# Performance work log

Hardware: AMD Instinct MI355X
Metric: run time of the kernel (lower is better)

## Reference

```python
import jax, jax.numpy as jnp
import numpy as np

N_NODES = 200000
D = 128            # in_channels
B_GRAPHS = 512     # batch_size
STEPS = 3          # processing_steps


def setup_inputs() -> dict:
    key = jax.random.key(0)
    k = jax.random.split(key, 6)
    x = jax.random.normal(k[0], (N_NODES, D), dtype=jnp.float32)
    batch = jnp.sort(jax.random.randint(k[1], (N_NODES,), 0, B_GRAPHS, dtype=jnp.int64))
    s = 0.1
    W_ih = jax.random.normal(k[2], (3 * D, 2 * D), dtype=jnp.float32) * s
    W_hh = jax.random.normal(k[3], (3 * D, D), dtype=jnp.float32) * s
    b_ih = jax.random.normal(k[4], (3 * D,), dtype=jnp.float32) * s
    b_hh = jax.random.normal(k[5], (3 * D,), dtype=jnp.float32) * s
    return {"x": x, "batch": batch, "batch_size": B_GRAPHS,
            "W_ih": W_ih, "W_hh": W_hh, "b_ih": b_ih, "b_hh": b_hh}


def _gru_cell(inp, h, W_ih, W_hh, b_ih, b_hh):
    # inp: [B, 2d], h: [B, d]; PyTorch GRU gate order: r, z, n
    gi = inp @ W_ih.T + b_ih  # [B, 3d]
    gh = h @ W_hh.T + b_hh    # [B, 3d]
    gi_r, gi_z, gi_n = jnp.split(gi, 3, axis=-1)
    gh_r, gh_z, gh_n = jnp.split(gh, 3, axis=-1)
    r = jax.nn.sigmoid(gi_r + gh_r)
    z = jax.nn.sigmoid(gi_z + gh_z)
    n = jnp.tanh(gi_n + r * gh_n)
    return (1.0 - z) * n + z * h


def reference(x, batch, batch_size, W_ih, W_hh, b_ih, b_hh):
    B = batch_size
    d = x.shape[1]
    h = jnp.zeros((B, d), dtype=x.dtype)
    q_star = jnp.zeros((B, 2 * d), dtype=x.dtype)
    for _ in range(STEPS):
        h = _gru_cell(q_star, h, W_ih, W_hh, b_ih, b_hh)
        q = h  # num_layers=1: output == new hidden state
        e = jnp.sum(x * q[batch], axis=-1)  # [N]
        m = jax.ops.segment_max(e, batch, num_segments=B)
        ex = jnp.exp(e - m[batch])
        s = jax.ops.segment_sum(ex, batch, num_segments=B)
        a = ex / (s[batch] + 1e-16)  # segment softmax weights [N]
        r = jax.ops.segment_sum(a[:, None] * x, batch, num_segments=B)  # [B, d]
        q_star = jnp.concatenate([q, r], axis=-1)
    return q_star
```

## Files before the change

kernel.cpp:

```cpp
#include <hip/hip_runtime.h>
#include <math.h>
#include <float.h>

constexpr int D = 128;
constexpr int B = 512;
constexpr int STEPS = 3;
constexpr int NW_IH = 3 * D * 2 * D;
constexpr int NW_HH = 3 * D * D;
constexpr float NEG_HUGE = -3.402823466e38f;

__device__ __forceinline__ float sigmoidf_(float x) { return 1.f / (1.f + __expf(-x)); }
__device__ __forceinline__ float bflo(unsigned int u) { return __uint_as_float(u << 16); }
__device__ __forceinline__ float bfhi(unsigned int u) { return __uint_as_float(u & 0xffff0000u); }
__device__ __forceinline__ unsigned short f2bf_rn(float f) {
    unsigned int u = __float_as_uint(f);
    u += 0x7fffu + ((u >> 16) & 1u);
    return (unsigned short)(u >> 16);
}
__device__ __forceinline__ float4 ld4(const float* p) { return *(const float4*)p; }
__device__ __forceinline__ int imin_(int a, int b) { return a < b ? a : b; }

__global__ __launch_bounds__(256) void k_prep(const float* __restrict__ Wih,
        const float* __restrict__ Whh, const int* __restrict__ batch, int n,
        unsigned short* __restrict__ wih_bf, unsigned short* __restrict__ whh_bf,
        int* __restrict__ seg) {
    int i = blockIdx.x * blockDim.x + threadIdx.x;
    if (i < NW_IH) wih_bf[i] = f2bf_rn(Wih[i]);
    else if (i < NW_IH + NW_HH) whh_bf[i - NW_IH] = f2bf_rn(Whh[i - NW_IH]);
    if (i <= B) {
        int lo = 0, hi = n;
        while (lo < hi) { int mid = (lo + hi) >> 1; if (batch[mid] < i) lo = mid + 1; else hi = mid; }
        seg[i] = lo;
    }
}

struct Trip { float4 a0, a1, b0, b1, c0, c1, d0, d1; };

__global__ __launch_bounds__(256, 2) void k_set2set(
        const float* __restrict__ x,
        const unsigned short* __restrict__ wih_bf,
        const unsigned short* __restrict__ whh_bf,
        const float* __restrict__ bih, const float* __restrict__ bhh,
        const int* __restrict__ seg, float* __restrict__ out) {
    __shared__ __align__(16) float s_q[2 * D];
    __shared__ __align__(16) float s_h[D];
    __shared__ float s_gi[3 * D], s_gh[3 * D];
    __shared__ float sm[16], sl[16];
    __shared__ __align__(16) float rpart[4][D];

    const int b = blockIdx.x;
    const int tid = threadIdx.x;
    const int start = seg[b], end = seg[b + 1];
    const int g = tid >> 4;
    const int s = tid & 15;
    const int s8 = s * 8;

    const int len = end - start;
    const int FT = (len + 63) >> 6;
    const int gbase = start + g;
    const int eclamp = (len > 0) ? end - 1 : start;

    float m_run, l_run;
    float4 acc0, acc1;
    float4 q0, q1;
    Trip T0_, T1_, T2_, T3_;

    auto load_trip = [&](Trip& T, int t) {
        const int n0 = gbase + (t << 6);
        const float* p0 = x + ((size_t)imin_(n0,      eclamp) << 7) + s8;
        const float* p1 = x + ((size_t)imin_(n0 + 16, eclamp) << 7) + s8;
        const float* p2 = x + ((size_t)imin_(n0 + 32, eclamp) << 7) + s8;
        const float* p3 = x + ((size_t)imin_(n0 + 48, eclamp) << 7) + s8;
        T.a0 = ld4(p0); T.a1 = ld4(p0 + 4);
        T.b0 = ld4(p1); T.b1 = ld4(p1 + 4);
        T.c0 = ld4(p2); T.c1 = ld4(p2 + 4);
        T.d0 = ld4(p3); T.d1 = ld4(p3 + 4);
    };
    auto dot8 = [&](const float4& lo, const float4& hi) {
        float p = lo.x * q0.x;
        p = fmaf(lo.y, q0.y, p); p = fmaf(lo.z, q0.z, p); p = fmaf(lo.w, q0.w, p);
        p = fmaf(hi.x, q1.x, p); p = fmaf(hi.y, q1.y, p);
        p = fmaf(hi.z, q1.z, p); p = fmaf(hi.w, q1.w, p);
        return p;
    };
    auto compute_core = [&](const Trip& T, bool masked, int t) {
        float p0 = dot8(T.a0, T.a1);
        float p1 = dot8(T.b0, T.b1);
        float p2 = dot8(T.c0, T.c1);
        float p3 = dot8(T.d0, T.d1);
        p0 += __shfl_xor(p0, 1, 64); p1 += __shfl_xor(p1, 1, 64);
        p2 += __shfl_xor(p2, 1, 64); p3 += __shfl_xor(p3, 1, 64);
        p0 += __shfl_xor(p0, 2, 64); p1 += __shfl_xor(p1, 2, 64);
        p2 += __shfl_xor(p2, 2, 64); p3 += __shfl_xor(p3, 2, 64);
        p0 += __shfl_xor(p0, 4, 64); p1 += __shfl_xor(p1, 4, 64);
        p2 += __shfl_xor(p2, 4, 64); p3 += __shfl_xor(p3, 4, 64);
        p0 += __shfl_xor(p0, 8, 64); p1 += __shfl_xor(p1, 8, 64);
        p2 += __shfl_xor(p2, 8, 64); p3 += __shfl_xor(p3, 8, 64);
        bool m0 = true, m1 = true, m2 = true, m3 = true;
        float h0 = p0, h1 = p1, h2 = p2, h3 = p3;
        if (masked) {
            const int n0 = gbase + (t << 6);
            m0 = n0 < end; m1 = n0 + 16 < end; m2 = n0 + 32 < end; m3 = n0 + 48 < end;
            h0 = m0 ? p0 : NEG_HUGE; h1 = m1 ? p1 : NEG_HUGE;
            h2 = m2 ? p2 : NEG_HUGE; h3 = m3 ? p3 : NEG_HUGE;
        }
        float nm = fmaxf(m_run, fmaxf(fmaxf(h0, h1), fmaxf(h2, h3)));
        float sc = __expf(m_run - nm);
        float e0 = __expf(p0 - nm), e1 = __expf(p1 - nm);
        float e2 = __expf(p2 - nm), e3 = __expf(p3 - nm);
        if (masked) {
            e0 = m0 ? e0 : 0.f; e1 = m1 ? e1 : 0.f;
            e2 = m2 ? e2 : 0.f; e3 = m3 ? e3 : 0.f;
        }
        l_run = fmaf(l_run, sc, (e0 + e1) + (e2 + e3));
        acc0.x = fmaf(acc0.x, sc, fmaf(e0, T.a0.x, fmaf(e1, T.b0.x, fmaf(e2, T.c0.x, e3 * T.d0.x))));
        acc0.y = fmaf(acc0.y, sc, fmaf(e0, T.a0.y, fmaf(e1, T.b0.y, fmaf(e2, T.c0.y, e3 * T.d0.y))));
        acc0.z = fmaf(acc0.z, sc, fmaf(e0, T.a0.z, fmaf(e1, T.b0.z, fmaf(e2, T.c0.z, e3 * T.d0.z))));
        acc0.w = fmaf(acc0.w, sc, fmaf(e0, T.a0.w, fmaf(e1, T.b0.w, fmaf(e2, T.c0.w, e3 * T.d0.w))));
        acc1.x = fmaf(acc1.x, sc, fmaf(e0, T.a1.x, fmaf(e1, T.b1.x, fmaf(e2, T.c1.x, e3 * T.d1.x))));
        acc1.y = fmaf(acc1.y, sc, fmaf(e0, T.a1.y, fmaf(e1, T.b1.y, fmaf(e2, T.c1.y, e3 * T.d1.y))));
        acc1.z = fmaf(acc1.z, sc, fmaf(e0, T.a1.z, fmaf(e1, T.b1.z, fmaf(e2, T.c1.z, e3 * T.d1.z))));
        acc1.w = fmaf(acc1.w, sc, fmaf(e0, T.a1.w, fmaf(e1, T.b1.w, fmaf(e2, T.c1.w, e3 * T.d1.w))));
        m_run = nm;
    };
    auto compute  = [&](const Trip& T)        { compute_core(T, false, 0); };
    auto computeM = [&](const Trip& T, int t) { compute_core(T, true,  t); };

    if (FT > 0) load_trip(T0_, 0);
    if (FT > 1) load_trip(T1_, 1);
    if (FT > 2) load_trip(T2_, 2);
    if (FT > 3) load_trip(T3_, 3);

    if (tid < 2 * D) s_q[tid] = 0.f;
    if (tid < D) s_h[tid] = 0.f;
    __syncthreads();

    for (int step = 0; step < STEPS; ++step) {
        if (tid < 192) {
            const int r0 = tid * 2, r1 = r0 + 1;
            float gi0 = bih[r0], gi1 = bih[r1];
            float gh0 = bhh[r0], gh1 = bhh[r1];
            const float4* q4 = (const float4*)s_q;
            const float4* h4 = (const float4*)s_h;
            const uint4* w0 = (const uint4*)(wih_bf + (size_t)r0 * (2 * D));
            const uint4* w1 = (const uint4*)(wih_bf + (size_t)r1 * (2 * D));
#pragma unroll 4
            for (int c = 0; c < 32; ++c) {
                uint4 wa = w0[c], wb = w1[c];
                float4 qa = q4[2 * c], qb = q4[2 * c + 1];
                gi0 = fmaf(bflo(wa.x), qa.x, gi0); gi0 = fmaf(bfhi(wa.x), qa.y, gi0);
                gi0 = fmaf(bflo(wa.y), qa.z, gi0); gi0 = fmaf(bfhi(wa.y), qa.w, gi0);
                gi0 = fmaf(bflo(wa.z), qb.x, gi0); gi0 = fmaf(bfhi(wa.z), qb.y, gi0);
                gi0 = fmaf(bflo(wa.w), qb.z, gi0); gi0 = fmaf(bfhi(wa.w), qb.w, gi0);
                gi1 = fmaf(bflo(wb.x), qa.x, gi1); gi1 = fmaf(bfhi(wb.x), qa.y, gi1);
                gi1 = fmaf(bflo(wb.y), qa.z, gi1); gi1 = fmaf(bfhi(wb.y), qa.w, gi1);
                gi1 = fmaf(bflo(wb.z), qb.x, gi1); gi1 = fmaf(bfhi(wb.z), qb.y, gi1);
                gi1 = fmaf(bflo(wb.w), qb.z, gi1); gi1 = fmaf(bfhi(wb.w), qb.w, gi1);
            }
            const uint4* v0 = (const uint4*)(whh_bf + (size_t)r0 * D);
            const uint4* v1 = (const uint4*)(whh_bf + (size_t)r1 * D);
#pragma unroll 4
            for (int c = 0; c < 16; ++c) {
                uint4 wa = v0[c], wb = v1[c];
                float4 ha = h4[2 * c], hb = h4[2 * c + 1];
                gh0 = fmaf(bflo(wa.x), ha.x, gh0); gh0 = fmaf(bfhi(wa.x), ha.y, gh0);
                gh0 = fmaf(bflo(wa.y), ha.z, gh0); gh0 = fmaf(bfhi(wa.y), ha.w, gh0);
                gh0 = fmaf(bflo(wa.z), hb.x, gh0); gh0 = fmaf(bfhi(wa.z), hb.y, gh0);
                gh0 = fmaf(bflo(wa.w), hb.z, gh0); gh0 = fmaf(bfhi(wa.w), hb.w, gh0);
                gh1 = fmaf(bflo(wb.x), ha.x, gh1); gh1 = fmaf(bfhi(wb.x), ha.y, gh1);
                gh1 = fmaf(bflo(wb.y), ha.z, gh1); gh1 = fmaf(bfhi(wb.y), ha.w, gh1);
                gh1 = fmaf(bflo(wb.z), hb.x, gh1); gh1 = fmaf(bfhi(wb.z), hb.y, gh1);
                gh1 = fmaf(bflo(wb.w), hb.z, gh1); gh1 = fmaf(bfhi(wb.w), hb.w, gh1);
            }
            s_gi[r0] = gi0; s_gi[r1] = gi1;
            s_gh[r0] = gh0; s_gh[r1] = gh1;
        }
        __syncthreads();
        if (tid < D) {
            const int t = tid;
            float r  = sigmoidf_(s_gi[t] + s_gh[t]);
            float z  = sigmoidf_(s_gi[D + t] + s_gh[D + t]);
            float nn = tanhf(s_gi[2 * D + t] + r * s_gh[2 * D + t]);
            float hn = (1.f - z) * nn + z * s_h[t];
            s_h[t] = hn;
            s_q[t] = hn;
        }
        __syncthreads();

        q0 = ((const float4*)s_h)[2 * s];
        q1 = ((const float4*)s_h)[2 * s + 1];
        m_run = NEG_HUGE; l_run = 0.f;
        acc0 = make_float4(0.f, 0.f, 0.f, 0.f);
        acc1 = make_float4(0.f, 0.f, 0.f, 0.f);

        int t = 0;
        while (t + 8 <= FT) {
            compute(T0_); load_trip(T0_, t + 4);
            compute(T1_); load_trip(T1_, t + 5);
            compute(T2_); load_trip(T2_, t + 6);
            compute(T3_); load_trip(T3_, t + 7);
            t += 4;
        }
        int rem = FT - t;
        if (rem > 4) {
            compute(T0_); load_trip(T0_, t + 4);
            compute(T1_); if (rem > 5) load_trip(T1_, t + 5);
            compute(T2_); if (rem > 6) load_trip(T2_, t + 6);
            compute(T3_);
            t += 4; rem -= 4;
        }
        if (rem > 0) { if (t     == FT - 1) computeM(T0_, t);     else compute(T0_); }
        if (rem > 1) { if (t + 1 == FT - 1) computeM(T1_, t + 1); else compute(T1_); }
        if (rem > 2) { if (t + 2 == FT - 1) computeM(T2_, t + 2); else compute(T2_); }
        if (rem > 3) computeM(T3_, t + 3);

        if (step + 1 < STEPS) {
            if (FT > 0) load_trip(T0_, 0);
            if (FT > 1) load_trip(T1_, 1);
            if (FT > 2) load_trip(T2_, 2);
            if (FT > 3) load_trip(T3_, 3);
        }

        if (s == 0) { sm[g] = m_run; sl[g] = l_run; }
        __syncthreads();

        {
            const float mv = sm[s];
            const float lv = sl[s];
            float M = mv;
            M = fmaxf(M, __shfl_xor(M, 1, 64));
            M = fmaxf(M, __shfl_xor(M, 2, 64));
            M = fmaxf(M, __shfl_xor(M, 4, 64));
            M = fmaxf(M, __shfl_xor(M, 8, 64));
            float term = lv * __expf(mv - M);
            term += __shfl_xor(term, 1, 64);
            term += __shfl_xor(term, 2, 64);
            term += __shfl_xor(term, 4, 64);
            term += __shfl_xor(term, 8, 64);
            const float inv = 1.f / (term + 1e-16f);
            const float fac = __expf(m_run - M) * inv;
            acc0.x *= fac; acc0.y *= fac; acc0.z *= fac; acc0.w *= fac;
            acc1.x *= fac; acc1.y *= fac; acc1.z *= fac; acc1.w *= fac;
        }
        acc0.x += __shfl_xor(acc0.x, 16, 64); acc0.y += __shfl_xor(acc0.y, 16, 64);
        acc0.z += __shfl_xor(acc0.z, 16, 64); acc0.w += __shfl_xor(acc0.w, 16, 64);
        acc1.x += __shfl_xor(acc1.x, 16, 64); acc1.y += __shfl_xor(acc1.y, 16, 64);
        acc1.z += __shfl_xor(acc1.z, 16, 64); acc1.w += __shfl_xor(acc1.w, 16, 64);
        acc0.x += __shfl_xor(acc0.x, 32, 64); acc0.y += __shfl_xor(acc0.y, 32, 64);
        acc0.z += __shfl_xor(acc0.z, 32, 64); acc0.w += __shfl_xor(acc0.w, 32, 64);
        acc1.x += __shfl_xor(acc1.x, 32, 64); acc1.y += __shfl_xor(acc1.y, 32, 64);
        acc1.z += __shfl_xor(acc1.z, 32, 64); acc1.w += __shfl_xor(acc1.w, 32, 64);

        const int wv = tid >> 6;
        if ((tid & 63) < 16) {
            float4* dst = (float4*)&rpart[wv][s8];
            dst[0] = acc0; dst[1] = acc1;
        }
        __syncthreads();
        if (tid < D) {
            float v = (rpart[0][tid] + rpart[1][tid]) + (rpart[2][tid] + rpart[3][tid]);
            s_q[D + tid] = v;
        }
        __syncthreads();
    }

    if (tid < 2 * D) out[(size_t)b * (2 * D) + tid] = s_q[tid];
}

extern "C" void kernel_launch(void* const* d_in, const int* in_sizes, int n_in,
                              void* d_out, int out_size, void* d_ws, size_t ws_size,
                              hipStream_t stream) {
    const float* x    = (const float*)d_in[0];
    const int*   batch= (const int*)d_in[1];
    const float* Wih  = (const float*)d_in[3];
    const float* Whh  = (const float*)d_in[4];
    const float* bih  = (const float*)d_in[5];
    const float* bhh  = (const float*)d_in[6];
    const int n = in_sizes[0] / D;

    char* ws = (char*)d_ws;
    int* seg = (int*)ws;
    unsigned short* wih_bf = (unsigned short*)(ws + 4096);
    unsigned short* whh_bf = (unsigned short*)(ws + 4096 + (size_t)NW_IH * 2);

    const int total = NW_IH + NW_HH;
    k_prep<<<(total + 255) / 256, 256, 0, stream>>>(Wih, Whh, batch, n, wih_bf, whh_bf, seg);
    k_set2set<<<B, 256, 0, stream>>>(x, wih_bf, whh_bf, bih, bhh, seg, (float*)d_out);
}
```

Baseline: 268.3 us.

## Parallelize GRU matvec across all lanes, coalesce x loads, shrink prefetch depth

The GRU gate matvecs move from 192 threads each computing two full rows serially to all 256 threads, with half-wave or quarter-wave lanes splitting each row and reducing via shuffles. Biases are added in the elementwise stage. The x row loads switch from 8 contiguous floats per lane to two 16-byte loads 64 floats apart, so each load instruction is contiguous across lanes. The prefetch ring drops from four to two trips, freeing registers but exposing more memory latency on large segments, and the first trip is now loaded each step before the GRU instead of overlapped with the previous step's tail.

Result: slower. 335.0 us (+24.9%).

```diff
diff --git a/kernel.cpp b/kernel.cpp
--- a/kernel.cpp
+++ b/kernel.cpp
@@ -53,7 +53,7 @@
     const int start = seg[b], end = seg[b + 1];
     const int g = tid >> 4;
     const int s = tid & 15;
-    const int s8 = s * 8;
+    const int s4 = s * 4;
 
     const int len = end - start;
     const int FT = (len + 63) >> 6;
@@ -63,18 +63,18 @@
     float m_run, l_run;
     float4 acc0, acc1;
     float4 q0, q1;
-    Trip T0_, T1_, T2_, T3_;
+    Trip T0_, T1_;
 
     auto load_trip = [&](Trip& T, int t) {
         const int n0 = gbase + (t << 6);
-        const float* p0 = x + ((size_t)imin_(n0,      eclamp) << 7) + s8;
-        const float* p1 = x + ((size_t)imin_(n0 + 16, eclamp) << 7) + s8;
-        const float* p2 = x + ((size_t)imin_(n0 + 32, eclamp) << 7) + s8;
-        const float* p3 = x + ((size_t)imin_(n0 + 48, eclamp) << 7) + s8;
-        T.a0 = ld4(p0); T.a1 = ld4(p0 + 4);
-        T.b0 = ld4(p1); T.b1 = ld4(p1 + 4);
-        T.c0 = ld4(p2); T.c1 = ld4(p2 + 4);
-        T.d0 = ld4(p3); T.d1 = ld4(p3 + 4);
+        const float* p0 = x + ((size_t)imin_(n0,      eclamp) << 7) + s4;
+        const float* p1 = x + ((size_t)imin_(n0 + 16, eclamp) << 7) + s4;
+        const float* p2 = x + ((size_t)imin_(n0 + 32, eclamp) << 7) + s4;
+        const float* p3 = x + ((size_t)imin_(n0 + 48, eclamp) << 7) + s4;
+        T.a0 = ld4(p0); T.a1 = ld4(p0 + 64);
+        T.b0 = ld4(p1); T.b1 = ld4(p1 + 64);
+        T.c0 = ld4(p2); T.c1 = ld4(p2 + 64);
+        T.d0 = ld4(p3); T.d1 = ld4(p3 + 64);
     };
     auto dot8 = [&](const float4& lo, const float4& hi) {
         float p = lo.x * q0.x;
@@ -126,99 +126,98 @@
     auto compute  = [&](const Trip& T)        { compute_core(T, false, 0); };
     auto computeM = [&](const Trip& T, int t) { compute_core(T, true,  t); };
 
-    if (FT > 0) load_trip(T0_, 0);
-    if (FT > 1) load_trip(T1_, 1);
-    if (FT > 2) load_trip(T2_, 2);
-    if (FT > 3) load_trip(T3_, 3);
-
     if (tid < 2 * D) s_q[tid] = 0.f;
     if (tid < D) s_h[tid] = 0.f;
     __syncthreads();
 
+    const int wv   = tid >> 6;
+    const int l64  = tid & 63;
+    const int half = l64 >> 5, c32 = l64 & 31;
+    const int quarter = l64 >> 4, c16 = l64 & 15;
+    const int rb = wv * 96;
+
     for (int step = 0; step < STEPS; ++step) {
-        if (tid < 192) {
-            const int r0 = tid * 2, r1 = r0 + 1;
-            float gi0 = bih[r0], gi1 = bih[r1];
-            float gh0 = bhh[r0], gh1 = bhh[r1];
+        if (FT > 0) load_trip(T0_, 0);
+
+        {
             const float4* q4 = (const float4*)s_q;
             const float4* h4 = (const float4*)s_h;
-            const uint4* w0 = (const uint4*)(wih_bf + (size_t)r0 * (2 * D));
-            const uint4* w1 = (const uint4*)(wih_bf + (size_t)r1 * (2 * D));
-#pragma unroll 4
-            for (int c = 0; c < 32; ++c) {
-                uint4 wa = w0[c], wb = w1[c];
-                float4 qa = q4[2 * c], qb = q4[2 * c + 1];
-                gi0 = fmaf(bflo(wa.x), qa.x, gi0); gi0 = fmaf(bfhi(wa.x), qa.y, gi0);
-                gi0 = fmaf(bflo(wa.y), qa.z, gi0); gi0 = fmaf(bfhi(wa.y), qa.w, gi0);
-                gi0 = fmaf(bflo(wa.z), qb.x, gi0); gi0 = fmaf(bfhi(wa.z), qb.y, gi0);
-                gi0 = fmaf(bflo(wa.w), qb.z, gi0); gi0 = fmaf(bfhi(wa.w), qb.w, gi0);
-                gi1 = fmaf(bflo(wb.x), qa.x, gi1); gi1 = fmaf(bfhi(wb.x), qa.y, gi1);
-                gi1 = fmaf(bflo(wb.y), qa.z, gi1); gi1 = fmaf(bfhi(wb.y), qa.w, gi1);
-                gi1 = fmaf(bflo(wb.z), qb.x, gi1); gi1 = fmaf(bfhi(wb.z), qb.y, gi1);
-                gi1 = fmaf(bflo(wb.w), qb.z, gi1); gi1 = fmaf(bfhi(wb.w), qb.w, gi1);
+            const float4 qa = q4[c32 * 2], qb = q4[c32 * 2 + 1];
+            const float4 ha = h4[c16 * 2], hb = h4[c16 * 2 + 1];
+
+            for (int i = 0; i < 48; i += 2) {
+                const int rA = rb + 2 * i + half;
+                const int rB = rA + 2;
+                uint4 wA = *(const uint4*)(wih_bf + ((size_t)rA << 8) + c32 * 8);
+                uint4 wB = *(const uint4*)(wih_bf + ((size_t)rB << 8) + c32 * 8);
+                float pA = bflo(wA.x) * qa.x;
+                pA = fmaf(bfhi(wA.x), qa.y, pA); pA = fmaf(bflo(wA.y), qa.z, pA);
+                pA = fmaf(bfhi(wA.y), qa.w, pA); pA = fmaf(bflo(wA.z), qb.x, pA);
+                pA = fmaf(bfhi(wA.z), qb.y, pA); pA = fmaf(bflo(wA.w), qb.z, pA);
+                pA = fmaf(bfhi(wA.w), qb.w, pA);
+                float pB = bflo(wB.x) * qa.x;
+                pB = fmaf(bfhi(wB.x), qa.y, pB); pB = fmaf(bflo(wB.y), qa.z, pB);
+                pB = fmaf(bfhi(wB.y), qa.w, pB); pB = fmaf(bflo(wB.z), qb.x, pB);
+                pB = fmaf(bfhi(wB.z), qb.y, pB); pB = fmaf(bflo(wB.w), qb.z, pB);
+                pB = fmaf(bfhi(wB.w), qb.w, pB);
+                pA += __shfl_xor(pA, 1, 64);  pB += __shfl_xor(pB, 1, 64);
+                pA += __shfl_xor(pA, 2, 64);  pB += __shfl_xor(pB, 2, 64);
+                pA += __shfl_xor(pA, 4, 64);  pB += __shfl_xor(pB, 4, 64);
+                pA += __shfl_xor(pA, 8, 64);  pB += __shfl_xor(pB, 8, 64);
+                pA += __shfl_xor(pA, 16, 64); pB += __shfl_xor(pB, 16, 64);
+                if (c32 == 0) { s_gi[rA] = pA; s_gi[rB] = pB; }
             }
-            const uint4* v0 = (const uint4*)(whh_bf + (size_t)r0 * D);
-            const uint4* v1 = (const uint4*)(whh_bf + (size_t)r1 * D);
-#pragma unroll 4
-            for (int c = 0; c < 16; ++c) {
-                uint4 wa = v0[c], wb = v1[c];
-                float4 ha = h4[2 * c], hb = h4[2 * c + 1];
-                gh0 = fmaf(bflo(wa.x), ha.x, gh0); gh0 = fmaf(bfhi(wa.x), ha.y, gh0);
-                gh0 = fmaf(bflo(wa.y), ha.z, gh0); gh0 = fmaf(bfhi(wa.y), ha.w, gh0);
-                gh0 = fmaf(bflo(wa.z), hb.x, gh0); gh0 = fmaf(bfhi(wa.z), hb.y, gh0);
-                gh0 = fmaf(bflo(wa.w), hb.z, gh0); gh0 = fmaf(bfhi(wa.w), hb.w, gh0);
-                gh1 = fmaf(bflo(wb.x), ha.x, gh1); gh1 = fmaf(bfhi(wb.x), ha.y, gh1);
-                gh1 = fmaf(bflo(wb.y), ha.z, gh1); gh1 = fmaf(bfhi(wb.y), ha.w, gh1);
-                gh1 = fmaf(bflo(wb.z), hb.x, gh1); gh1 = fmaf(bfhi(wb.z), hb.y, gh1);
-                gh1 = fmaf(bflo(wb.w), hb.z, gh1); gh1 = fmaf(bfhi(wb.w), hb.w, gh1);
+            for (int j = 0; j < 24; j += 2) {
+                const int rA = rb + 4 * j + quarter;
+                const int rB = rA + 4;
+                uint4 wA = *(const uint4*)(whh_bf + ((size_t)rA << 7) + c16 * 8);
+                uint4 wB = *(const uint4*)(whh_bf + ((size_t)rB << 7) + c16 * 8);
+                float pA = bflo(wA.x) * ha.x;
+                pA = fmaf(bfhi(wA.x), ha.y, pA); pA = fmaf(bflo(wA.y), ha.z, pA);
+                pA = fmaf(bfhi(wA.y), ha.w, pA); pA = fmaf(bflo(wA.z), hb.x, pA);
+                pA = fmaf(bfhi(wA.z), hb.y, pA); pA = fmaf(bflo(wA.w), hb.z, pA);
+                pA = fmaf(bfhi(wA.w), hb.w, pA);
+                float pB = bflo(wB.x) * ha.x;
+                pB = fmaf(bfhi(wB.x), ha.y, pB); pB = fmaf(bflo(wB.y), ha.z, pB);
+                pB = fmaf(bfhi(wB.y), ha.w, pB); pB = fmaf(bflo(wB.z), hb.x, pB);
+                pB = fmaf(bfhi(wB.z), hb.y, pB); pB = fmaf(bflo(wB.w), hb.z, pB);
+                pB = fmaf(bfhi(wB.w), hb.w, pB);
+                pA += __shfl_xor(pA, 1, 64); pB += __shfl_xor(pB, 1, 64);
+                pA += __shfl_xor(pA, 2, 64); pB += __shfl_xor(pB, 2, 64);
+                pA += __shfl_xor(pA, 4, 64); pB += __shfl_xor(pB, 4, 64);
+                pA += __shfl_xor(pA, 8, 64); pB += __shfl_xor(pB, 8, 64);
+                if (c16 == 0) { s_gh[rA] = pA; s_gh[rB] = pB; }
             }
-            s_gi[r0] = gi0; s_gi[r1] = gi1;
-            s_gh[r0] = gh0; s_gh[r1] = gh1;
         }
         __syncthreads();
         if (tid < D) {
             const int t = tid;
-            float r  = sigmoidf_(s_gi[t] + s_gh[t]);
-            float z  = sigmoidf_(s_gi[D + t] + s_gh[D + t]);
-            float nn = tanhf(s_gi[2 * D + t] + r * s_gh[2 * D + t]);
+            float r  = sigmoidf_((s_gi[t] + bih[t]) + (s_gh[t] + bhh[t]));
+            float z  = sigmoidf_((s_gi[D + t] + bih[D + t]) + (s_gh[D + t] + bhh[D + t]));
+            float gin = s_gi[2 * D + t] + bih[2 * D + t];
+            float ghn = s_gh[2 * D + t] + bhh[2 * D + t];
+            float nn = tanhf(fmaf(r, ghn, gin));
             float hn = (1.f - z) * nn + z * s_h[t];
             s_h[t] = hn;
             s_q[t] = hn;
         }
         __syncthreads();
 
-        q0 = ((const float4*)s_h)[2 * s];
-        q1 = ((const float4*)s_h)[2 * s + 1];
+        q0 = ((const float4*)s_h)[s];
+        q1 = ((const float4*)s_h)[16 + s];
         m_run = NEG_HUGE; l_run = 0.f;
         acc0 = make_float4(0.f, 0.f, 0.f, 0.f);
         acc1 = make_float4(0.f, 0.f, 0.f, 0.f);
 
-        int t = 0;
-        while (t + 8 <= FT) {
-            compute(T0_); load_trip(T0_, t + 4);
-            compute(T1_); load_trip(T1_, t + 5);
-            compute(T2_); load_trip(T2_, t + 6);
-            compute(T3_); load_trip(T3_, t + 7);
-            t += 4;
-        }
-        int rem = FT - t;
-        if (rem > 4) {
-            compute(T0_); load_trip(T0_, t + 4);
-            compute(T1_); if (rem > 5) load_trip(T1_, t + 5);
-            compute(T2_); if (rem > 6) load_trip(T2_, t + 6);
-            compute(T3_);
-            t += 4; rem -= 4;
-        }
-        if (rem > 0) { if (t     == FT - 1) computeM(T0_, t);     else compute(T0_); }
-        if (rem > 1) { if (t + 1 == FT - 1) computeM(T1_, t + 1); else compute(T1_); }
-        if (rem > 2) { if (t + 2 == FT - 1) computeM(T2_, t + 2); else compute(T2_); }
-        if (rem > 3) computeM(T3_, t + 3);
-
-        if (step + 1 < STEPS) {
-            if (FT > 0) load_trip(T0_, 0);
+        if (FT > 0) {
             if (FT > 1) load_trip(T1_, 1);
-            if (FT > 2) load_trip(T2_, 2);
-            if (FT > 3) load_trip(T3_, 3);
+            int t = 0;
+            for (; t + 2 < FT; t += 2) {
+                compute(T0_); load_trip(T0_, t + 2);
+                compute(T1_); if (t + 3 < FT) load_trip(T1_, t + 3);
+            }
+            if (t == FT - 1) computeM(T0_, t);
+            else { compute(T0_); computeM(T1_, t + 1); }
         }
 
         if (s == 0) { sm[g] = m_run; sl[g] = l_run; }
@@ -251,10 +250,9 @@
         acc1.x += __shfl_xor(acc1.x, 32, 64); acc1.y += __shfl_xor(acc1.y, 32, 64);
         acc1.z += __shfl_xor(acc1.z, 32, 64); acc1.w += __shfl_xor(acc1.w, 32, 64);
 
-        const int wv = tid >> 6;
-        if ((tid & 63) < 16) {
-            float4* dst = (float4*)&rpart[wv][s8];
-            dst[0] = acc0; dst[1] = acc1;
+        if (l64 < 16) {
+            *(float4*)&rpart[wv][s4]      = acc0;
+            *(float4*)&rpart[wv][64 + s4] = acc1;
         }
         __syncthreads();
         if (tid < D) {
```

## Cut register prefetch depth to two trips, coalesce loads, skip step-0 GEMV

Applied to the files above, without the earlier changes.

Each thread's two float4 loads from a node row now sit 64 floats apart instead of being adjacent. This makes a 16-lane group read contiguous 256-byte spans per load. The prefetch pipeline drops from four in-flight trips to two and is restarted at the top of each step, which frees registers for occupancy at the cost of less latency hiding. The first-step GRU matrix-vector products are replaced by copying the biases, since q_star and h are zero then.

After: 220.0 us. -18.0%, faster.

```diff
diff --git a/kernel.cpp b/kernel.cpp
--- a/kernel.cpp
+++ b/kernel.cpp
@@ -53,7 +53,7 @@
     const int start = seg[b], end = seg[b + 1];
     const int g = tid >> 4;
     const int s = tid & 15;
-    const int s8 = s * 8;
+    const int s4 = s * 4;
 
     const int len = end - start;
     const int FT = (len + 63) >> 6;
@@ -63,18 +63,18 @@
     float m_run, l_run;
     float4 acc0, acc1;
     float4 q0, q1;
-    Trip T0_, T1_, T2_, T3_;
+    Trip T0_, T1_;
 
     auto load_trip = [&](Trip& T, int t) {
         const int n0 = gbase + (t << 6);
-        const float* p0 = x + ((size_t)imin_(n0,      eclamp) << 7) + s8;
-        const float* p1 = x + ((size_t)imin_(n0 + 16, eclamp) << 7) + s8;
-        const float* p2 = x + ((size_t)imin_(n0 + 32, eclamp) << 7) + s8;
-        const float* p3 = x + ((size_t)imin_(n0 + 48, eclamp) << 7) + s8;
-        T.a0 = ld4(p0); T.a1 = ld4(p0 + 4);
-        T.b0 = ld4(p1); T.b1 = ld4(p1 + 4);
-        T.c0 = ld4(p2); T.c1 = ld4(p2 + 4);
-        T.d0 = ld4(p3); T.d1 = ld4(p3 + 4);
+        const float* p0 = x + ((size_t)imin_(n0,      eclamp) << 7) + s4;
+        const float* p1 = x + ((size_t)imin_(n0 + 16, eclamp) << 7) + s4;
+        const float* p2 = x + ((size_t)imin_(n0 + 32, eclamp) << 7) + s4;
+        const float* p3 = x + ((size_t)imin_(n0 + 48, eclamp) << 7) + s4;
+        T.a0 = ld4(p0); T.a1 = ld4(p0 + 64);
+        T.b0 = ld4(p1); T.b1 = ld4(p1 + 64);
+        T.c0 = ld4(p2); T.c1 = ld4(p2 + 64);
+        T.d0 = ld4(p3); T.d1 = ld4(p3 + 64);
     };
     auto dot8 = [&](const float4& lo, const float4& hi) {
         float p = lo.x * q0.x;
@@ -126,17 +126,16 @@
     auto compute  = [&](const Trip& T)        { compute_core(T, false, 0); };
     auto computeM = [&](const Trip& T, int t) { compute_core(T, true,  t); };
 
-    if (FT > 0) load_trip(T0_, 0);
-    if (FT > 1) load_trip(T1_, 1);
-    if (FT > 2) load_trip(T2_, 2);
-    if (FT > 3) load_trip(T3_, 3);
-
     if (tid < 2 * D) s_q[tid] = 0.f;
     if (tid < D) s_h[tid] = 0.f;
     __syncthreads();
 
     for (int step = 0; step < STEPS; ++step) {
-        if (tid < 192) {
+        if (FT > 0) load_trip(T0_, 0);
+
+        if (step == 0) {
+            for (int i = tid; i < 3 * D; i += 256) { s_gi[i] = bih[i]; s_gh[i] = bhh[i]; }
+        } else if (tid < 192) {
             const int r0 = tid * 2, r1 = r0 + 1;
             float gi0 = bih[r0], gi1 = bih[r1];
             float gh0 = bhh[r0], gh1 = bhh[r1];
@@ -187,38 +186,21 @@
         }
         __syncthreads();
 
-        q0 = ((const float4*)s_h)[2 * s];
-        q1 = ((const float4*)s_h)[2 * s + 1];
+        q0 = ((const float4*)s_h)[s];
+        q1 = ((const float4*)s_h)[16 + s];
         m_run = NEG_HUGE; l_run = 0.f;
         acc0 = make_float4(0.f, 0.f, 0.f, 0.f);
         acc1 = make_float4(0.f, 0.f, 0.f, 0.f);
 
-        int t = 0;
-        while (t + 8 <= FT) {
-            compute(T0_); load_trip(T0_, t + 4);
-            compute(T1_); load_trip(T1_, t + 5);
-            compute(T2_); load_trip(T2_, t + 6);
-            compute(T3_); load_trip(T3_, t + 7);
-            t += 4;
-        }
-        int rem = FT - t;
-        if (rem > 4) {
-            compute(T0_); load_trip(T0_, t + 4);
-            compute(T1_); if (rem > 5) load_trip(T1_, t + 5);
-            compute(T2_); if (rem > 6) load_trip(T2_, t + 6);
-            compute(T3_);
-            t += 4; rem -= 4;
-        }
-        if (rem > 0) { if (t     == FT - 1) computeM(T0_, t);     else compute(T0_); }
-        if (rem > 1) { if (t + 1 == FT - 1) computeM(T1_, t + 1); else compute(T1_); }
-        if (rem > 2) { if (t + 2 == FT - 1) computeM(T2_, t + 2); else compute(T2_); }
-        if (rem > 3) computeM(T3_, t + 3);
-
-        if (step + 1 < STEPS) {
-            if (FT > 0) load_trip(T0_, 0);
+        if (FT > 0) {
             if (FT > 1) load_trip(T1_, 1);
-            if (FT > 2) load_trip(T2_, 2);
-            if (FT > 3) load_trip(T3_, 3);
+            int t = 0;
+            for (; t + 2 < FT; t += 2) {
+                compute(T0_); load_trip(T0_, t + 2);
+                compute(T1_); if (t + 3 < FT) load_trip(T1_, t + 3);
+            }
+            if (t == FT - 1) computeM(T0_, t);
+            else { compute(T0_); computeM(T1_, t + 1); }
         }
 
         if (s == 0) { sm[g] = m_run; sl[g] = l_run; }
@@ -253,8 +235,8 @@
 
         const int wv = tid >> 6;
         if ((tid & 63) < 16) {
-            float4* dst = (float4*)&rpart[wv][s8];
-            dst[0] = acc0; dst[1] = acc1;
+            *(float4*)&rpart[wv][s4]      = acc0;
+            *(float4*)&rpart[wv][64 + s4] = acc1;
         }
         __syncthreads();
         if (tid < D) {
```
